# Optimization experiments

Measured on AMD Instinct MI355X. Metric: run time of the kernel, lower is better.

## Reference

```python
import jax, jax.numpy as jnp
import numpy as np

N, D, TOP_K = 200000, 256, 1024
L = 64
EPS = 1e-8  # matches F.cosine_similarity eps


def setup_inputs() -> dict:
    key = jax.random.key(0)
    k1, k2, k3, k4, k5 = jax.random.split(key, 5)
    return {
        "node_embeddings": jax.random.normal(k1, (N, D), dtype=jnp.float32),
        "dist_table": jax.random.normal(k2, (3, 2), dtype=jnp.float32),       # nn.Embedding(3,2)
        "W": jax.random.normal(k3, (D, D + 2), dtype=jnp.float32) / np.sqrt(D + 2),  # Linear(d+2->d, no bias)
        "distance_tensor": jax.random.randint(k4, (N,), 0, 4),
        "label_node_idx": jax.random.randint(k5, (L,), 0, N),
        "source_node_idx": 12345,
    }


def reference(node_embeddings, dist_table, W, distance_tensor, label_node_idx, source_node_idx):
    # distance encoding lookup: clamp(dist-1, 0, 2)
    d_idx = jnp.clip(distance_tensor.astype(jnp.int32) - 1, 0, 2)
    denc = dist_table[d_idx]                                         # [N, 2]
    x = jnp.concatenate([node_embeddings, denc], axis=1)             # [N, D+2]
    transformed = x @ W.T                                            # [N, D]

    # cosine similarity of source embedding vs all transformed embeddings
    q = node_embeddings[source_node_idx]                             # [D]
    qn = q / jnp.maximum(jnp.linalg.norm(q), EPS)
    tn = transformed / jnp.maximum(
        jnp.linalg.norm(transformed, axis=1, keepdims=True), EPS)
    cos = tn @ qn                                                    # [N]

    # validity mask and distance weights (1.0 / 1.5 / 2.0)
    valid = distance_tensor <= 2
    w = jnp.where(distance_tensor == 1, 1.5,
                  jnp.where(distance_tensor == 2, 2.0, 1.0)).astype(cos.dtype)
    weighted = jnp.where(valid, cos * w, -jnp.inf)                   # invalid -> never selected
    _, topk_idx = jax.lax.top_k(weighted, TOP_K)                     # N_valid >> TOP_K here

    # softmax-style retrieval loss: sum_labels (logsumexp(all.q) - label.q)
    logits = transformed @ q                                         # [N]
    lse = jax.nn.logsumexp(logits)
    loss = jnp.sum(lse - logits[label_node_idx])

    # final_top_k = unique(topk U one-hop U source); fixed-shape boolean membership mask
    mask = jnp.zeros((N,), dtype=bool).at[topk_idx].set(True)
    mask = mask | (distance_tensor == 1) | (jnp.arange(N) == source_node_idx)
    return loss, mask
```

## Files before the change

### kernel.cpp

```cpp
#include <hip/hip_runtime.h>
#include <math.h>

#define D 256
#define TOPK 1024
#define EPS 1e-8f

typedef __attribute__((ext_vector_type(8))) short short8;
typedef __attribute__((ext_vector_type(4))) float f32x4;

__device__ __forceinline__ unsigned encf(float f){
  unsigned b = __float_as_uint(f);
  return b ^ ((unsigned)((int)b >> 31) | 0x80000000u);
}
__device__ __forceinline__ float decf(unsigned u){
  unsigned b = (u & 0x80000000u) ? (u ^ 0x80000000u) : ~u;
  return __uint_as_float(b);
}

__device__ __forceinline__ void gload16(const void* g, void* l){
  __builtin_amdgcn_global_load_lds(
      (const __attribute__((address_space(1))) unsigned*)g,
      (__attribute__((address_space(3))) unsigned*)l, 16, 0, 0);
}

__global__ __launch_bounds__(256) void k1_setup(
    const float* __restrict__ emb, const float* __restrict__ dtab,
    const float* __restrict__ W, const int* __restrict__ srcp,
    short* __restrict__ Wbs, float* __restrict__ WD, float* __restrict__ QN,
    unsigned* __restrict__ SC, unsigned* __restrict__ ZB, int N)
{
  int tid = threadIdx.x;
  int blk = blockIdx.x;
  if (blk == 0 && tid == 0){
    SC[0]=0u;
    ((float*)SC)[1]=0.0f;
    SC[2]=0u;
    SC[3]=0u;
    SC[4]=(unsigned)TOPK;
  }
  if (blk < 256){
    int c = blk;
    int k = tid;
    float f = W[(size_t)c*258 + k];
    unsigned u  = __float_as_uint(f);
    unsigned hb = u & 0xffff0000u;
    float r = f - __uint_as_float(hb);
    unsigned mb = __float_as_uint(r) & 0xffff0000u;
    float r2 = r - __uint_as_float(mb);
    unsigned lb = __float_as_uint(r2) & 0xffff0000u;
    int q = c >> 6, colq = c & 63, cf = colq >> 4, c0 = colq & 15;
    int ch = k >> 5, kk = k & 31, g = kk >> 3, e = kk & 7;
    size_t idx0 = (size_t)q*49152 + ((size_t)(ch*3)*4 + cf)*512 + (g*16 + c0)*8 + e;
    Wbs[idx0       ] = (short)(hb>>16);
    Wbs[idx0 + 2048] = (short)(mb>>16);
    Wbs[idx0 + 4096] = (short)(lb>>16);
  } else if (blk == 256){
    int k = tid;
    float w6 = W[(size_t)k*258 + 256], w7 = W[(size_t)k*258 + 257];
    WD[k]     = w6*dtab[0] + w7*dtab[1];
    WD[256+k] = w6*dtab[2] + w7*dtab[3];
    WD[512+k] = w6*dtab[4] + w7*dtab[5];
    int src = srcp[0];
    float qk = emb[(size_t)src*D + k];
    __shared__ float red[256];
    red[tid]=qk*qk; __syncthreads();
    for (int s2=128;s2>0;s2>>=1){ if (tid<s2) red[tid]+=red[tid+s2]; __syncthreads(); }
    if (tid==0) QN[0] = sqrtf(red[0]);
  } else {
    unsigned zid = (unsigned)(blk-257)*256u + (unsigned)tid;
    if (zid < 6144u + 2u*(unsigned)N) ZB[zid] = 0u;
  }
}

#define SPLIT(x0,x1, AH,AM,AL) do{ float xs[8]={x0.x,x0.y,x0.z,x0.w,x1.x,x1.y,x1.z,x1.w}; \
  _Pragma("unroll") for(int _e=0;_e<8;++_e){ float _f=xs[_e]; unsigned _u=__float_as_uint(_f); \
    unsigned _hb=_u&0xffff0000u; float _r=_f-__uint_as_float(_hb); \
    unsigned _mb=__float_as_uint(_r)&0xffff0000u; float _r2=_r-__uint_as_float(_mb); \
    unsigned _lb=__float_as_uint(_r2)&0xffff0000u; \
    AH[_e]=(short)(_hb>>16); AM[_e]=(short)(_mb>>16); AL[_e]=(short)(_lb>>16);} }while(0)

#define READB(S_) do{ _Pragma("unroll") for (int _cf=0;_cf<4;++_cf) \
  b[_cf] = *(const short8*)(Bsh + ((ch*3+(S_))*4+_cf)*512 + (lane<<3)); }while(0)

#define MFMA_PASS(ASPL) do{ _Pragma("unroll") for (int _rf=0;_rf<4;++_rf){ \
  _Pragma("unroll") for (int _cf=0;_cf<4;++_cf) \
    acc[_rf][_cf] = __builtin_amdgcn_mfma_f32_16x16x32_bf16(ASPL[_rf], b[_cf], acc[_rf][_cf],0,0,0); } }while(0)

__global__ __launch_bounds__(512,2) void k2_main(
    const float* __restrict__ emb, const int* __restrict__ dist,
    const int* __restrict__ srcp, const short* __restrict__ Wbs,
    const float* __restrict__ WD, float* __restrict__ Sg,
    float* __restrict__ Qg, int N)
{
  extern __shared__ short Bsh[];
  int tid = threadIdx.x;
  int wave = tid >> 6;
  int lane = tid & 63;
  int g = lane >> 4;
  int c0 = lane & 15;

  int q  = blockIdx.x & 3;
  int rb = blockIdx.x >> 2;
  int RPB = (N + 63) >> 6;
  int rstart = rb * RPB;
  int rend = rstart + RPB; if (rend > N) rend = N;
  int ITERS = (RPB + 511) >> 9;

  const char* Wq = (const char*)(Wbs + (size_t)q*49152);
  #pragma unroll
  for (int i=0;i<12;++i){
    int off = (i*512 + tid)*16;
    gload16(Wq + off, (char*)Bsh + off);
  }

  int colbase = q*64;
  float qq[4], wdq0[4], wdq1[4], wdq2[4];
  {
    int src = srcp[0];
    #pragma unroll
    for (int cf=0;cf<4;++cf){
      int col = colbase + cf*16 + c0;
      qq[cf]   = emb[(size_t)src*D + col];
      wdq0[cf] = WD[col];
      wdq1[cf] = WD[256+col];
      wdq2[cf] = WD[512+col];
    }
  }
  __syncthreads();

  for (int it=0; it<ITERS; ++it){
    int rowbase = rstart + it*512 + wave*64;
    const float* xp0; const float* xp1; const float* xp2; const float* xp3;
    {
      int r0 = rowbase + c0;        xp0 = emb + (size_t)(r0<N? r0 : N-1)*D + 8*g;
      int r1 = rowbase + 16 + c0;   xp1 = emb + (size_t)(r1<N? r1 : N-1)*D + 8*g;
      int r2 = rowbase + 32 + c0;   xp2 = emb + (size_t)(r2<N? r2 : N-1)*D + 8*g;
      int r3 = rowbase + 48 + c0;   xp3 = emb + (size_t)(r3<N? r3 : N-1)*D + 8*g;
    }
    f32x4 acc[4][4];
    #pragma unroll
    for (int rf=0;rf<4;++rf)
      #pragma unroll
      for (int cf=0;cf<4;++cf) acc[rf][cf] = (f32x4){0.f,0.f,0.f,0.f};

    float4 xc[4][2], xn[4][2];
    xc[0][0]=*(const float4*)(xp0); xc[0][1]=*(const float4*)(xp0+4);
    xc[1][0]=*(const float4*)(xp1); xc[1][1]=*(const float4*)(xp1+4);
    xc[2][0]=*(const float4*)(xp2); xc[2][1]=*(const float4*)(xp2+4);
    xc[3][0]=*(const float4*)(xp3); xc[3][1]=*(const float4*)(xp3+4);

    for (int ch=0; ch<8; ++ch){
      if (ch < 7){
        int o = 32*(ch+1);
        xn[0][0]=*(const float4*)(xp0+o); xn[0][1]=*(const float4*)(xp0+o+4);
        xn[1][0]=*(const float4*)(xp1+o); xn[1][1]=*(const float4*)(xp1+o+4);
        xn[2][0]=*(const float4*)(xp2+o); xn[2][1]=*(const float4*)(xp2+o+4);
        xn[3][0]=*(const float4*)(xp3+o); xn[3][1]=*(const float4*)(xp3+o+4);
      }
      short8 ah[4], am[4], al[4];
      #pragma unroll
      for (int rf=0;rf<4;++rf) SPLIT(xc[rf][0], xc[rf][1], ah[rf], am[rf], al[rf]);

      short8 b[4];
      READB(0);
      MFMA_PASS(ah);
      MFMA_PASS(am);
      MFMA_PASS(al);
      READB(1);
      MFMA_PASS(ah);
      MFMA_PASS(am);
      READB(2);
      MFMA_PASS(ah);

      if (ch < 7){
        #pragma unroll
        for (int rf=0;rf<4;++rf){ xc[rf][0]=xn[rf][0]; xc[rf][1]=xn[rf][1]; }
      }
    }

    #pragma unroll
    for (int rf=0; rf<4; ++rf){
      #pragma unroll
      for (int r=0;r<4;++r){
        int row = rowbase + rf*16 + 4*g + r;
        bool wr = (row < rend);
        int dv = wr ? dist[row] : 3;
        int di = dv-1; di = di<0?0:(di>2?2:di);
        float S=0.f, Q=0.f;
        #pragma unroll
        for (int cf=0;cf<4;++cf){
          float wd = (di==0)? wdq0[cf] : (di==1)? wdq1[cf] : wdq2[cf];
          float v = acc[rf][cf][r] + wd;
          S = fmaf(v, qq[cf], S);
          Q = fmaf(v, v, Q);
        }
        #pragma unroll
        for (int off=1; off<16; off<<=1){
          S += __shfl_xor(S, off);
          Q += __shfl_xor(Q, off);
        }
        if (c0==0 && wr){
          atomicAdd(&Sg[row], S);
          atomicAdd(&Qg[row], Q);
        }
      }
    }
  }
}

__global__ __launch_bounds__(256) void k2b_enc(
    const int* __restrict__ dist, const float* __restrict__ Sg,
    const float* __restrict__ Qg, const float* __restrict__ QN,
    unsigned* __restrict__ UK, unsigned* __restrict__ SC,
    unsigned* __restrict__ H0, int N)
{
  __shared__ unsigned h[2048];
  int tid = threadIdx.x;
  int lane = tid & 63;
  for (int i=tid;i<2048;i+=256) h[i]=0u;
  __syncthreads();
  int n = blockIdx.x*256 + tid;
  float sval = -INFINITY;
  if (n < N){
    float S = Sg[n], Q = Qg[n];
    int dv = dist[n];
    float qn = QN[0];
    float den = fmaxf(sqrtf(Q), EPS) * fmaxf(qn, EPS);
    float cosv = S/den;
    float wgt = (dv==1)?1.5f:((dv==2)?2.0f:1.0f);
    float wv = (dv<=2)? cosv*wgt : -INFINITY;
    unsigned u = encf(wv);
    UK[n] = u;
    if (u > 0x007FFFFFu) atomicAdd(&h[u>>21],1u);
    sval = S;
  }
  float m = sval;
  #pragma unroll
  for (int off=32;off>0;off>>=1) m = fmaxf(m, __shfl_down(m, off));
  if (lane==0) atomicMax(&SC[0], encf(m));
  __syncthreads();
  for (int i=tid;i<2048;i+=256){ unsigned v=h[i]; if (v) atomicAdd(&H0[i], v); }
}

__global__ __launch_bounds__(256) void kh_hist(
    const unsigned* __restrict__ UK, const unsigned* __restrict__ SC,
    unsigned* __restrict__ Hp, int pass, int N)
{
  __shared__ unsigned h[2048];
  int bins = (pass==2)?1024:2048;
  int tid = threadIdx.x;
  for (int i=tid;i<bins;i+=256) h[i]=0u;
  __syncthreads();
  unsigned pfx = SC[3];
  int n = blockIdx.x*256 + tid;
  if (n < N){
    unsigned u = UK[n];
    bool incl; unsigned bin;
    if (pass==1){ incl = ((u>>21)==pfx); bin = (u>>10)&2047u; }
    else { incl = ((u>>10)==pfx); bin = u & 1023u; }
    if (incl) atomicAdd(&h[bin], 1u);
  }
  __syncthreads();
  for (int i=tid;i<bins;i+=256){ unsigned v=h[i]; if (v) atomicAdd(&Hp[i], v); }
}

__global__ __launch_bounds__(256) void ks_scan(
    const unsigned* __restrict__ Hp, unsigned* __restrict__ SC, int pass)
{
  __shared__ unsigned h[2048];
  __shared__ unsigned part[256];
  int bins=(pass==2)?1024:2048;
  int per = bins/256;
  int tid=threadIdx.x;
  unsigned ps=0;
  for (int i=0;i<per;++i){ unsigned v=Hp[tid*per+i]; h[tid*per+i]=v; ps+=v; }
  part[tid]=ps;
  __syncthreads();
  if (tid==0){
    unsigned Kp = SC[4];
    unsigned cum=0;
    int sc2=0;
    for (int t=255;t>=0;--t){
      if (cum + part[t] >= Kp){ sc2=t; break; }
      cum += part[t];
    }
    int sel = sc2*per;
    for (int b2=sc2*per+per-1; b2>=sc2*per; --b2){
      if (cum + h[b2] >= Kp){ sel=b2; break; }
      cum += h[b2];
    }
    SC[4] = Kp - cum;
    int bitsp = (pass==2)?10:11;
    SC[3] = (SC[3] << bitsp) | (unsigned)sel;
  }
}

__global__ __launch_bounds__(256) void k6_final(
    const int* __restrict__ dist, const int* __restrict__ srcp,
    const float* __restrict__ Sv, const unsigned* __restrict__ UK,
    unsigned* __restrict__ SC, unsigned* __restrict__ EQL,
    float* __restrict__ out, int N)
{
  int tid=threadIdx.x;
  int n=blockIdx.x*256+tid;
  unsigned T = SC[3];
  float M = decf(SC[0]);
  int src = srcp[0];
  float e=0.f;
  if (n<N){
    unsigned u = UK[n];
    int dv = dist[n];
    bool base = (u>T) || (dv==1) || (n==src);
    out[1+n] = base ? 1.0f : 0.0f;
    if (u==T){
      unsigned i = atomicAdd(&SC[2], 1u);
      if (i < 4096u) EQL[i] = (unsigned)n;
    }
    e = expf(Sv[n]-M);
  }
  __shared__ float red[256];
  red[tid]=e; __syncthreads();
  for (int st=128;st>0;st>>=1){ if (tid<st) red[tid]+=red[tid+st]; __syncthreads(); }
  if (tid==0) atomicAdd((float*)&SC[1], red[0]);
}

__global__ __launch_bounds__(256) void k7_loss(
    const int* __restrict__ labels, const float* __restrict__ Sv,
    unsigned* __restrict__ SC, const unsigned* __restrict__ EQL,
    float* __restrict__ out, int L)
{
  __shared__ float red[256];
  __shared__ unsigned lst[4096];
  int tid=threadIdx.x;
  float v=0.f;
  if (tid<L) v = Sv[labels[tid]];
  red[tid]=v; __syncthreads();
  for (int st=128;st>0;st>>=1){ if (tid<st) red[tid]+=red[tid+st]; __syncthreads(); }
  if (tid==0){
    float M = decf(SC[0]);
    float se = ((const float*)SC)[1];
    out[0] = (float)L*(M + logf(se)) - red[0];
  }
  unsigned cnt = SC[2]; if (cnt>4096u) cnt=4096u;
  unsigned quota = SC[4];
  for (unsigned i=tid;i<cnt;i+=256u) lst[i]=EQL[i];
  __syncthreads();
  if (cnt <= quota){
    for (unsigned i=tid;i<cnt;i+=256u) out[1+lst[i]] = 1.0f;
  } else {
    for (unsigned i=tid;i<cnt;i+=256u){
      unsigned me=lst[i]; unsigned rank=0;
      for (unsigned j=0;j<cnt;++j) rank += (lst[j]<me)?1u:0u;
      if (rank<quota) out[1+me]=1.0f;
    }
  }
}

extern "C" void kernel_launch(void* const* d_in, const int* in_sizes, int n_in,
                              void* d_out, int out_size, void* d_ws, size_t ws_size,
                              hipStream_t stream)
{
  const float* emb  = (const float*)d_in[0];
  const float* dtab = (const float*)d_in[1];
  const float* W    = (const float*)d_in[2];
  const int* dist   = (const int*)d_in[3];
  const int* labels = (const int*)d_in[4];
  const int* srcp   = (const int*)d_in[5];
  float* out = (float*)d_out;
  int N = in_sizes[3];
  int L = in_sizes[4];

  float* ws = (float*)d_ws;
  short* Wbs = (short*)ws;
  float* WD  = (float*)(Wbs + 196608);
  float* QN  = WD + 768;
  unsigned* SC = (unsigned*)(QN + 1);
  unsigned* H0 = SC + 8;
  unsigned* H1 = H0 + 2048;
  unsigned* H2 = H1 + 2048;
  float* Sg = (float*)(H2 + 2048);
  float* Qg = Sg + N;
  unsigned* UK = (unsigned*)(Qg + N);
  unsigned* EQL = UK + N;

  static bool lds_inited = false;
  if (!lds_inited){
    hipFuncSetAttribute((const void*)k2_main,
                        hipFuncAttributeMaxDynamicSharedMemorySize, 98304);
    lds_inited = true;
  }

  int grid  = (N + 255)/256;
  int grid1 = 257 + (6144 + 2*N + 255)/256;
  k1_setup<<<grid1,256,0,stream>>>(emb, dtab, W, srcp, Wbs, WD, QN, SC, H0, N);
  k2_main<<<256,512,98304,stream>>>(emb, dist, srcp, Wbs, WD, Sg, Qg, N);
  k2b_enc<<<grid,256,0,stream>>>(dist, Sg, Qg, QN, UK, SC, H0, N);
  ks_scan<<<1,256,0,stream>>>(H0, SC, 0);
  kh_hist<<<grid,256,0,stream>>>(UK, SC, H1, 1, N);
  ks_scan<<<1,256,0,stream>>>(H1, SC, 1);
  kh_hist<<<grid,256,0,stream>>>(UK, SC, H2, 2, N);
  ks_scan<<<1,256,0,stream>>>(H2, SC, 2);
  k6_final<<<grid,256,0,stream>>>(dist, srcp, Sg, UK, SC, EQL, out, N);
  k7_loss<<<1,256,0,stream>>>(labels, Sg, SC, EQL, out, L);
}
```

Before: 507.6 us.

## Fuse encode/histogram into GEMM kernel via last-block counter and remap blocks per XCD

Removes the separate k2b_enc launch: each of the four column-quarter blocks covering a row range bumps a per-range counter, and the last one to finish reads the accumulated S/Q with atomics, encodes the keys, builds the top-level histogram and updates the max. Block indices are also remapped so the four quarter blocks sharing a row range land on the same XCD, which should improve L2 reuse of the embedding rows. The chunk loop is manually unrolled by two with ping-pong register buffers instead of copying xn into xc. In exchange it adds a threadfence, an extra sync and a serialized tail of work on the last block per range, and the workspace layout shifts to hold the counters.

```diff
diff --git a/kernel.cpp b/kernel.cpp
--- a/kernel.cpp
+++ b/kernel.cpp
@@ -68,7 +68,7 @@
     if (tid==0) QN[0] = sqrtf(red[0]);
   } else {
     unsigned zid = (unsigned)(blk-257)*256u + (unsigned)tid;
-    if (zid < 6144u + 2u*(unsigned)N) ZB[zid] = 0u;
+    if (zid < 6144u + 2u*(unsigned)N + 64u) ZB[zid] = 0u;
   }
 }
 
@@ -79,28 +79,49 @@
     unsigned _lb=__float_as_uint(_r2)&0xffff0000u; \
     AH[_e]=(short)(_hb>>16); AM[_e]=(short)(_mb>>16); AL[_e]=(short)(_lb>>16);} }while(0)
 
-#define READB(S_) do{ _Pragma("unroll") for (int _cf=0;_cf<4;++_cf) \
-  b[_cf] = *(const short8*)(Bsh + ((ch*3+(S_))*4+_cf)*512 + (lane<<3)); }while(0)
+#define READB(CH_, S_) do{ _Pragma("unroll") for (int _cf=0;_cf<4;++_cf) \
+  b[_cf] = *(const short8*)(Bsh + (((CH_)*3+(S_))*4+_cf)*512 + (lane<<3)); }while(0)
 
 #define MFMA_PASS(ASPL) do{ _Pragma("unroll") for (int _rf=0;_rf<4;++_rf){ \
   _Pragma("unroll") for (int _cf=0;_cf<4;++_cf) \
     acc[_rf][_cf] = __builtin_amdgcn_mfma_f32_16x16x32_bf16(ASPL[_rf], b[_cf], acc[_rf][_cf],0,0,0); } }while(0)
 
+#define LOADX(dst, off) do{ \
+  dst[0][0]=*(const float4*)(xp0+(off)); dst[0][1]=*(const float4*)(xp0+(off)+4); \
+  dst[1][0]=*(const float4*)(xp1+(off)); dst[1][1]=*(const float4*)(xp1+(off)+4); \
+  dst[2][0]=*(const float4*)(xp2+(off)); dst[2][1]=*(const float4*)(xp2+(off)+4); \
+  dst[3][0]=*(const float4*)(xp3+(off)); dst[3][1]=*(const float4*)(xp3+(off)+4); }while(0)
+
+#define CHUNK(XS, CH_) do{ \
+  short8 ah[4], am[4], al[4]; \
+  _Pragma("unroll") for (int _rf=0;_rf<4;++_rf) SPLIT(XS[_rf][0],XS[_rf][1],ah[_rf],am[_rf],al[_rf]); \
+  short8 b[4]; \
+  READB(CH_,0); MFMA_PASS(ah); MFMA_PASS(am); MFMA_PASS(al); \
+  READB(CH_,1); MFMA_PASS(ah); MFMA_PASS(am); \
+  READB(CH_,2); MFMA_PASS(ah); }while(0)
+
 __global__ __launch_bounds__(512,2) void k2_main(
     const float* __restrict__ emb, const int* __restrict__ dist,
     const int* __restrict__ srcp, const short* __restrict__ Wbs,
-    const float* __restrict__ WD, float* __restrict__ Sg,
-    float* __restrict__ Qg, int N)
+    const float* __restrict__ WD, const float* __restrict__ QN,
+    float* __restrict__ Sg, float* __restrict__ Qg,
+    unsigned* __restrict__ UK, unsigned* __restrict__ SC,
+    unsigned* __restrict__ H0, unsigned* __restrict__ QC, int N)
 {
   extern __shared__ short Bsh[];
+  __shared__ unsigned qcount;
   int tid = threadIdx.x;
   int wave = tid >> 6;
   int lane = tid & 63;
   int g = lane >> 4;
   int c0 = lane & 15;
 
-  int q  = blockIdx.x & 3;
-  int rb = blockIdx.x >> 2;
+  int bi = blockIdx.x;
+  int xcd = bi & 7;
+  int slot = bi >> 3;
+  int q = slot & 3;
+  int rbi = slot >> 2;
+  int rb = xcd*8 + rbi;
   int RPB = (N + 63) >> 6;
   int rstart = rb * RPB;
   int rend = rstart + RPB; if (rend > N) rend = N;
@@ -144,38 +165,12 @@
       for (int cf=0;cf<4;++cf) acc[rf][cf] = (f32x4){0.f,0.f,0.f,0.f};
 
     float4 xc[4][2], xn[4][2];
-    xc[0][0]=*(const float4*)(xp0); xc[0][1]=*(const float4*)(xp0+4);
-    xc[1][0]=*(const float4*)(xp1); xc[1][1]=*(const float4*)(xp1+4);
-    xc[2][0]=*(const float4*)(xp2); xc[2][1]=*(const float4*)(xp2+4);
-    xc[3][0]=*(const float4*)(xp3); xc[3][1]=*(const float4*)(xp3+4);
-
-    for (int ch=0; ch<8; ++ch){
-      if (ch < 7){
-        int o = 32*(ch+1);
-        xn[0][0]=*(const float4*)(xp0+o); xn[0][1]=*(const float4*)(xp0+o+4);
-        xn[1][0]=*(const float4*)(xp1+o); xn[1][1]=*(const float4*)(xp1+o+4);
-        xn[2][0]=*(const float4*)(xp2+o); xn[2][1]=*(const float4*)(xp2+o+4);
-        xn[3][0]=*(const float4*)(xp3+o); xn[3][1]=*(const float4*)(xp3+o+4);
-      }
-      short8 ah[4], am[4], al[4];
-      #pragma unroll
-      for (int rf=0;rf<4;++rf) SPLIT(xc[rf][0], xc[rf][1], ah[rf], am[rf], al[rf]);
-
-      short8 b[4];
-      READB(0);
-      MFMA_PASS(ah);
-      MFMA_PASS(am);
-      MFMA_PASS(al);
-      READB(1);
-      MFMA_PASS(ah);
-      MFMA_PASS(am);
-      READB(2);
-      MFMA_PASS(ah);
-
-      if (ch < 7){
-        #pragma unroll
-        for (int rf=0;rf<4;++rf){ xc[rf][0]=xn[rf][0]; xc[rf][1]=xn[rf][1]; }
-      }
+    LOADX(xc, 0);
+    for (int ch=0; ch<8; ch+=2){
+      LOADX(xn, 32*(ch+1));
+      CHUNK(xc, ch);
+      if (ch < 6) LOADX(xc, 32*(ch+2));
+      CHUNK(xn, ch+1);
     }
 
     #pragma unroll
@@ -206,40 +201,36 @@
       }
     }
   }
-}
-
-__global__ __launch_bounds__(256) void k2b_enc(
-    const int* __restrict__ dist, const float* __restrict__ Sg,
-    const float* __restrict__ Qg, const float* __restrict__ QN,
-    unsigned* __restrict__ UK, unsigned* __restrict__ SC,
-    unsigned* __restrict__ H0, int N)
-{
-  __shared__ unsigned h[2048];
-  int tid = threadIdx.x;
-  int lane = tid & 63;
-  for (int i=tid;i<2048;i+=256) h[i]=0u;
-  __syncthreads();
-  int n = blockIdx.x*256 + tid;
-  float sval = -INFINITY;
-  if (n < N){
-    float S = Sg[n], Q = Qg[n];
-    int dv = dist[n];
+
+  __threadfence();
+  __syncthreads();
+  if (tid == 0) qcount = atomicAdd(&QC[rb], 1u);
+  __syncthreads();
+  if (qcount == 3u){
+    unsigned* h = (unsigned*)Bsh;
+    for (int i=tid;i<2048;i+=512) h[i]=0u;
+    __syncthreads();
+    float mloc = -INFINITY;
     float qn = QN[0];
-    float den = fmaxf(sqrtf(Q), EPS) * fmaxf(qn, EPS);
-    float cosv = S/den;
-    float wgt = (dv==1)?1.5f:((dv==2)?2.0f:1.0f);
-    float wv = (dv<=2)? cosv*wgt : -INFINITY;
-    unsigned u = encf(wv);
-    UK[n] = u;
-    if (u > 0x007FFFFFu) atomicAdd(&h[u>>21],1u);
-    sval = S;
-  }
-  float m = sval;
-  #pragma unroll
-  for (int off=32;off>0;off>>=1) m = fmaxf(m, __shfl_down(m, off));
-  if (lane==0) atomicMax(&SC[0], encf(m));
-  __syncthreads();
-  for (int i=tid;i<2048;i+=256){ unsigned v=h[i]; if (v) atomicAdd(&H0[i], v); }
+    for (int r = rstart + tid; r < rend; r += 512){
+      float S = atomicAdd(&Sg[r], 0.0f);
+      float Q = atomicAdd(&Qg[r], 0.0f);
+      int dv = dist[r];
+      float den = fmaxf(sqrtf(Q), EPS) * fmaxf(qn, EPS);
+      float cosv = S/den;
+      float wgt = (dv==1)?1.5f:((dv==2)?2.0f:1.0f);
+      float wv = (dv<=2)? cosv*wgt : -INFINITY;
+      unsigned u = encf(wv);
+      UK[r] = u;
+      if (u > 0x007FFFFFu) atomicAdd(&h[u>>21],1u);
+      mloc = fmaxf(mloc, S);
+    }
+    #pragma unroll
+    for (int off=32;off>0;off>>=1) mloc = fmaxf(mloc, __shfl_down(mloc, off));
+    if (lane==0) atomicMax(&SC[0], encf(mloc));
+    __syncthreads();
+    for (int i=tid;i<2048;i+=512){ unsigned v=h[i]; if (v) atomicAdd(&H0[i], v); }
+  }
 }
 
 __global__ __launch_bounds__(256) void kh_hist(
@@ -380,7 +371,8 @@
   unsigned* H2 = H1 + 2048;
   float* Sg = (float*)(H2 + 2048);
   float* Qg = Sg + N;
-  unsigned* UK = (unsigned*)(Qg + N);
+  unsigned* QC = (unsigned*)(Qg + N);
+  unsigned* UK = QC + 64;
   unsigned* EQL = UK + N;
 
   static bool lds_inited = false;
@@ -391,10 +383,9 @@
   }
 
   int grid  = (N + 255)/256;
-  int grid1 = 257 + (6144 + 2*N + 255)/256;
+  int grid1 = 257 + (6144 + 2*N + 64 + 255)/256;
   k1_setup<<<grid1,256,0,stream>>>(emb, dtab, W, srcp, Wbs, WD, QN, SC, H0, N);
-  k2_main<<<256,512,98304,stream>>>(emb, dist, srcp, Wbs, WD, Sg, Qg, N);
-  k2b_enc<<<grid,256,0,stream>>>(dist, Sg, Qg, QN, UK, SC, H0, N);
+  k2_main<<<256,512,98304,stream>>>(emb, dist, srcp, Wbs, WD, QN, Sg, Qg, UK, SC, H0, QC, N);
   ks_scan<<<1,256,0,stream>>>(H0, SC, 0);
   kh_hist<<<grid,256,0,stream>>>(UK, SC, H1, 1, N);
   ks_scan<<<1,256,0,stream>>>(H1, SC, 1);
```

After: 523.3 us. +3.1%, slower.
